# Performance work log

Measured on AMD Instinct MI355X. Metric: run time of the kernel, lower is better.

Reference implementation:

```python
import jax, jax.numpy as jnp
import numpy as np
from jax import lax

KH, KW, K = 3, 3, 9
PAD, BN_EPS = 1, 1e-5


def setup_inputs() -> dict:
    key = jax.random.key(0)
    ks = jax.random.split(key, 10)
    B, CHI, CHO, H, W = 2, 64, 64, 128, 128
    x = jax.random.normal(ks[0], (B, CHI, H, W), dtype=jnp.float32)
    # offset/mask branch conv: 3*K output channels (o1, o2, mask)
    w_off = jax.random.normal(ks[1], (3 * K, CHI, KH, KW), dtype=jnp.float32) * 0.01
    b_off = jax.random.normal(ks[2], (3 * K,), dtype=jnp.float32) * 0.01
    # main deformable conv weight/bias
    fan = CHI * K
    weight = jax.random.normal(ks[3], (CHO, CHI, KH, KW), dtype=jnp.float32) / np.sqrt(fan)
    bias = jax.random.normal(ks[4], (CHO,), dtype=jnp.float32) * 0.01
    # BatchNorm (eval-mode) params
    gamma = jax.random.uniform(ks[5], (CHO,), minval=0.5, maxval=1.5, dtype=jnp.float32)
    beta = jax.random.normal(ks[6], (CHO,), dtype=jnp.float32) * 0.1
    run_mean = jax.random.normal(ks[7], (CHO,), dtype=jnp.float32) * 0.1
    run_var = jax.random.uniform(ks[8], (CHO,), minval=0.5, maxval=1.5, dtype=jnp.float32)
    return {"x": x, "w_off": w_off, "b_off": b_off, "weight": weight,
            "bias": bias, "gamma": gamma, "beta": beta,
            "run_mean": run_mean, "run_var": run_var}


def _dcn_bn_relu(x, w_off, b_off, weight, bias, gamma, beta, run_mean, run_var):
    B, C, H, W = x.shape
    CHO = weight.shape[0]
    # offset/mask branch: regular 3x3 conv, stride 1, pad 1
    om = lax.conv_general_dilated(
        x, w_off, window_strides=(1, 1), padding=[(PAD, PAD), (PAD, PAD)],
        dimension_numbers=("NCHW", "OIHW", "NCHW")) + b_off[None, :, None, None]
    o1, o2, m = jnp.split(om, 3, axis=1)          # each [B, K, H, W]
    offset = jnp.concatenate([o1, o2], axis=1)    # [B, 2K, H, W]
    off_y = offset[:, 0::2]                       # interleaved (y, x) per tap, as in DCNv2 CUDA
    off_x = offset[:, 1::2]
    mask = jax.nn.sigmoid(m)                      # [B, K, H, W] modulation

    # sampling positions: p = p0 + p_k + offset
    ky, kx = jnp.meshgrid(jnp.arange(KH), jnp.arange(KW), indexing="ij")
    ky = ky.reshape(K).astype(x.dtype)
    kx = kx.reshape(K).astype(x.dtype)
    hh = jnp.arange(H, dtype=x.dtype)
    ww = jnp.arange(W, dtype=x.dtype)
    py = hh[None, None, :, None] - PAD + ky[None, :, None, None] + off_y  # [B,K,H,W]
    px = ww[None, None, None, :] - PAD + kx[None, :, None, None] + off_x

    y0f = jnp.floor(py)
    x0f = jnp.floor(px)
    ly = (py - y0f)[..., None]
    lx = (px - x0f)[..., None]
    y0 = y0f.astype(jnp.int32)
    x0 = x0f.astype(jnp.int32)
    bidx = jnp.arange(B)[:, None, None, None]

    def gather(yi, xi):
        valid = ((yi >= 0) & (yi < H) & (xi >= 0) & (xi < W)).astype(x.dtype)
        yc = jnp.clip(yi, 0, H - 1)
        xc = jnp.clip(xi, 0, W - 1)
        g = x[bidx, :, yc, xc]                    # [B, K, H, W, C]
        return g * valid[..., None]

    v00 = gather(y0, x0)
    v01 = gather(y0, x0 + 1)
    v10 = gather(y0 + 1, x0)
    v11 = gather(y0 + 1, x0 + 1)
    sampled = (v00 * (1 - ly) * (1 - lx) + v01 * (1 - ly) * lx
               + v10 * ly * (1 - lx) + v11 * ly * lx)
    sampled = sampled * mask[..., None]           # modulated

    out = jnp.einsum("bkhwc,ock->bohw", sampled,
                     weight.reshape(CHO, C, K)) + bias[None, :, None, None]

    # eval-mode BatchNorm + ReLU
    inv = gamma / jnp.sqrt(run_var + BN_EPS)
    out = (out - run_mean[None, :, None, None]) * inv[None, :, None, None] \
          + beta[None, :, None, None]
    return jax.nn.relu(out)


def reference(x, w_off, b_off, weight, bias, gamma, beta, run_mean, run_var):
    return _dcn_bn_relu(x, w_off, b_off, weight, bias, gamma, beta, run_mean, run_var)
```

## Files before the change

kernel.cpp:

```cpp
#include <hip/hip_runtime.h>
#include <hip/hip_bf16.h>

#define HH 128
#define WW 128
#define CI 64
#define CO 64
#define SLS 584
#define A_HPS 72
#define A_HW 66

typedef __attribute__((ext_vector_type(8))) short short8;
typedef __attribute__((ext_vector_type(4))) float floatx4;

__device__ __forceinline__ unsigned short f2bf(float f) {
  union { float f; unsigned u; } uu; uu.f = f;
  unsigned r = uu.u + 0x7FFFu + ((uu.u >> 16) & 1u);
  return (unsigned short)(r >> 16);
}
__device__ __forceinline__ unsigned pack2bf(float lo, float hi) {
  return (unsigned)f2bf(lo) | ((unsigned)f2bf(hi) << 16);
}

__global__ __launch_bounds__(256) void prep_kernel(
    const float* __restrict__ weight, const float* __restrict__ bias,
    const float* __restrict__ gamma, const float* __restrict__ beta,
    const float* __restrict__ mean, const float* __restrict__ var,
    const float* __restrict__ w_off, const float* __restrict__ b_off,
    unsigned short* __restrict__ Wm, unsigned short* __restrict__ w2,
    float* __restrict__ bias2, float* __restrict__ boff2) {
  int idx = blockIdx.x * 256 + threadIdx.x;
  if (idx < 32) boff2[idx] = (idx < 27) ? b_off[idx] : 0.f;
  if (idx >= CO * 576) return;
  int o = idx / 576, kc = idx - o * 576;
  int k = kc >> 6, c = kc & 63;
  float inv = gamma[o] * rsqrtf(var[o] + 1e-5f);
  Wm[idx] = f2bf(weight[(o * CI + c) * 9 + k] * inv);
  if (kc == 0) bias2[o] = (bias[o] - mean[o]) * inv + beta[o];
  if (o < 27) w2[idx] = f2bf(w_off[o * 576 + c * 9 + k]);
  else if (o < 32) w2[idx] = 0;
}

__global__ __launch_bounds__(256) void offA_kernel(
    const float* __restrict__ x, unsigned* __restrict__ xTb_u,
    const unsigned short* __restrict__ w2, const float* __restrict__ boff2,
    float* __restrict__ om32) {
  __shared__ short halo[3 * A_HW * A_HPS];
  int bid = blockIdx.x;
  int s = bid & 7;
  int n = bid >> 3;
  int b = n >> 5;
  int rest = n & 31;
  int h = s * 16 + (rest & 15);
  int w0 = (rest >> 4) * 64;
  int tid = threadIdx.x;

#pragma unroll
  for (int it = 0; it < 4; it++) {
    int t = it * 256 + tid;
    if (t < 792) {
      int row = t / 264;
      int r2 = t - row * 264;
      int cg4 = r2 / 66;
      int px = r2 - cg4 * 66;
      int y = h - 1 + row;
      int xi = w0 - 1 + px;
      int c0 = cg4 * 16;
      float f[16];
      if (((unsigned)y < (unsigned)HH) && ((unsigned)xi < (unsigned)WW)) {
        const float* xp = x + ((long)(b * CI + c0) * HH + y) * WW + xi;
#pragma unroll
        for (int q = 0; q < 16; q++) f[q] = xp[q * (HH * WW)];
      } else {
#pragma unroll
        for (int q = 0; q < 16; q++) f[q] = 0.f;
      }
      short* hp = &halo[(row * A_HW + px) * A_HPS + c0];
#pragma unroll
      for (int q = 0; q < 4; q++)
        *(uint2*)(hp + q * 4) =
            make_uint2(pack2bf(f[4 * q], f[4 * q + 1]), pack2bf(f[4 * q + 2], f[4 * q + 3]));
    }
  }
  __syncthreads();

  {
    int cp = tid & 31;
    int pw = tid >> 5;
#pragma unroll
    for (int it = 0; it < 8; it++) {
      int px = it * 8 + pw;
      unsigned u = *(const unsigned*)&halo[(A_HW + px + 1) * A_HPS + 2 * cp];
      xTb_u[((b * HH + h) * WW + w0 + px) * 32 + cp] = u;
    }
  }

  int lane = tid & 63, wave = tid >> 6;
  int r16 = lane & 15, quad = lane >> 4;
  int m16 = wave & 1;
  floatx4 binit = *(const floatx4*)(boff2 + m16 * 16 + quad * 4);
  const short* ap = (const short*)(w2 + (m16 * 16 + r16) * 576);
#pragma unroll
  for (int i = 0; i < 2; i++) {
    int nt = (wave >> 1) + 2 * i;
    floatx4 t = binit;
#pragma unroll
    for (int kk = 0; kk < 9; kk++) {
      int dy = kk / 3, dx = kk - 3 * (kk / 3);
      const short* hp = &halo[(dy * A_HW + nt * 16 + r16 + dx) * A_HPS];
      short8 b0 = *(const short8*)(hp + quad * 8);
      short8 b1 = *(const short8*)(hp + 32 + quad * 8);
      short8 a0 = *(const short8*)(ap + kk * 64 + quad * 8);
      short8 a1 = *(const short8*)(ap + kk * 64 + 32 + quad * 8);
      t = __builtin_amdgcn_mfma_f32_16x16x32_bf16(a0, b0, t, 0, 0, 0);
      t = __builtin_amdgcn_mfma_f32_16x16x32_bf16(a1, b1, t, 0, 0, 0);
    }
    float* orow = om32 + (long)((b * HH + h) * WW + w0 + nt * 16 + r16) * 32;
#pragma unroll
    for (int r = 0; r < 4; r++) {
      int oc = m16 * 16 + quad * 4 + r;
      if (oc < 27) orow[oc] = t[r];
    }
  }
}

__global__ __launch_bounds__(256) void dcnB_kernel(
    const unsigned short* __restrict__ xTb, const float* __restrict__ om32,
    const unsigned short* __restrict__ Wm, const float* __restrict__ bias2,
    float* __restrict__ out) {
  __shared__ __hip_bfloat16 SL[16 * SLS];
  __shared__ float4 Pw[144];
  __shared__ int2 Po[144];

  int bid = blockIdx.x;
  int s = bid & 7;
  int n = bid >> 3;
  int b = n >> 7;
  int rem = n & 127;
  int h = s * 16 + (rem >> 3);
  int w0 = (rem & 7) * 16;

  int tid = threadIdx.x, lane = tid & 63, wave = tid >> 6;
  const unsigned short* xb = xTb + b * (HH * WW * CI);
  int rowpix = (b * HH + h) * WW + w0;

  if (lane < 36) {
    int p_loc = (lane * 7282) >> 16;
    int k = lane - p_loc * 9;
    int p = wave * 4 + p_loc;
    const float* ob = om32 + (long)(rowpix + p) * 32;
    float oy = ob[2 * k], ox = ob[2 * k + 1], mm = ob[18 + k];
    float msk = 1.f / (1.f + __expf(-mm));
    int ky = (k * 11) >> 5;
    int kx = k - 3 * ky;
    float py = (float)(h - 1 + ky) + oy;
    float px = (float)(w0 + p - 1 + kx) + ox;
    float y0f = floorf(py), x0f = floorf(px);
    float ly = py - y0f, lx = px - x0f;
    int y0 = (int)y0f, x0 = (int)x0f;
    int y1 = y0 + 1, x1 = x0 + 1;
    float lylx = ly * lx;
    bool y0v = (unsigned)y0 < (unsigned)HH, y1v = (unsigned)y1 < (unsigned)HH;
    bool x0v = (unsigned)x0 < (unsigned)WW, x1v = (unsigned)x1 < (unsigned)WW;
    int yc0 = min(max(y0, 0), HH - 1), yc1 = min(max(y1, 0), HH - 1);
    int xc0 = min(max(x0, 0), WW - 1), xc1 = min(max(x1, 0), WW - 1);
    Pw[p * 9 + k] = make_float4((y0v && x0v) ? (1.f - ly - lx + lylx) * msk : 0.f,
                                (y0v && x1v) ? (lx - lylx) * msk : 0.f,
                                (y1v && x0v) ? (ly - lylx) * msk : 0.f,
                                (y1v && x1v) ? lylx * msk : 0.f);
    int dxs = (xc1 - xc0) * CI;
    int dys = (yc1 - yc0) * WW * CI;
    Po[p * 9 + k] = make_int2((yc0 * WW + xc0) * CI, dxs | (dys << 16));
  }

  int cp = lane & 31, ph = lane >> 5, ch = 2 * cp;
#pragma unroll
  for (int j = 0; j < 2; j++) {
    int p = wave * 4 + j * 2 + ph;
#pragma unroll
    for (int k = 0; k < 9; k++) {
      float4 wv = Pw[p * 9 + k];
      int2 po = Po[p * 9 + k];
      int o00 = po.x + ch;
      int dx = po.y & 0xffff;
      int dyv = po.y >> 16;
      unsigned u00 = *(const unsigned*)(xb + o00);
      unsigned u01 = *(const unsigned*)(xb + o00 + dx);
      unsigned u10 = *(const unsigned*)(xb + o00 + dyv);
      unsigned u11 = *(const unsigned*)(xb + o00 + dyv + dx);
      float lo = __uint_as_float(u00 << 16) * wv.x + __uint_as_float(u01 << 16) * wv.y +
                 __uint_as_float(u10 << 16) * wv.z + __uint_as_float(u11 << 16) * wv.w;
      float hi = __uint_as_float(u00 & 0xffff0000u) * wv.x + __uint_as_float(u01 & 0xffff0000u) * wv.y +
                 __uint_as_float(u10 & 0xffff0000u) * wv.z + __uint_as_float(u11 & 0xffff0000u) * wv.w;
      *(unsigned*)(&SL[p * SLS + k * 64 + ch]) = pack2bf(lo, hi);
    }
  }
  __syncthreads();

  int r16 = lane & 15, quad = lane >> 4;
  floatx4 acc = *(const floatx4*)(bias2 + wave * 16 + quad * 4);
  const unsigned short* Ap = Wm + (wave * 16 + r16) * 576 + quad * 8;
  const __hip_bfloat16* Sp = &SL[r16 * SLS + quad * 8];
#pragma unroll
  for (int kc0 = 0; kc0 < 576; kc0 += 32) {
    short8 av = *(const short8*)(Ap + kc0);
    short8 bv = *(const short8*)(Sp + kc0);
    acc = __builtin_amdgcn_mfma_f32_16x16x32_bf16(av, bv, acc, 0, 0, 0);
  }
#pragma unroll
  for (int r = 0; r < 4; r++) {
    int o = wave * 16 + quad * 4 + r;
    out[((b * CO + o) * HH + h) * WW + w0 + r16] = fmaxf(acc[r], 0.f);
  }
}

extern "C" void kernel_launch(void* const* d_in, const int* in_sizes, int n_in,
                              void* d_out, int out_size, void* d_ws, size_t ws_size,
                              hipStream_t stream) {
  const float* x = (const float*)d_in[0];
  const float* w_off = (const float*)d_in[1];
  const float* b_off = (const float*)d_in[2];
  const float* weight = (const float*)d_in[3];
  const float* bias = (const float*)d_in[4];
  const float* gamma = (const float*)d_in[5];
  const float* beta = (const float*)d_in[6];
  const float* run_mean = (const float*)d_in[7];
  const float* run_var = (const float*)d_in[8];
  float* outp = (float*)d_out;

  char* ws = (char*)d_ws;
  unsigned* xTb = (unsigned*)ws;
  float* om32 = (float*)(ws + 4194304);
  unsigned short* Wm = (unsigned short*)(ws + 8388608);
  unsigned short* w2 = (unsigned short*)(ws + 8462336);
  float* bias2 = (float*)(ws + 8499200);
  float* boff2 = (float*)(ws + 8499456);

  prep_kernel<<<144, 256, 0, stream>>>(weight, bias, gamma, beta, run_mean, run_var,
                                       w_off, b_off, Wm, w2, bias2, boff2);
  offA_kernel<<<512, 256, 0, stream>>>(x, xTb, w2, boff2, om32);
  dcnB_kernel<<<2048, 256, 0, stream>>>((const unsigned short*)xTb, om32, Wm, bias2, outp);
}
```

Measured before the change: 111.9 us.

## Fuse offset conv into DCN kernel and move x transpose into prep kernel

Removes the separate offset-conv kernel and its om32 buffer. The NHWC bf16 transpose of x now runs in extra blocks of the prep kernel through a shared-memory transpose. Each DCN block computes its own 3x3 offset/mask conv on a small 3x18-pixel halo loaded from xTb, splitting K across wave pairs, and keeps the result in shared memory that is aliased with the sampling buffer. This saves a launch and a global round-trip for the offsets, at the cost of recomputing halo loads per 16-pixel tile. The gather is also widened to 4 channels per lane.

After: 117.1 us. 4.6% more time.

```diff
diff --git a/kernel.cpp b/kernel.cpp
--- a/kernel.cpp
+++ b/kernel.cpp
@@ -6,8 +6,8 @@
 #define CI 64
 #define CO 64
 #define SLS 584
-#define A_HPS 72
-#define A_HW 66
+#define HPS 72
+#define HALW 18
 
 typedef __attribute__((ext_vector_type(8))) short short8;
 typedef __attribute__((ext_vector_type(4))) float floatx4;
@@ -20,15 +20,44 @@
 __device__ __forceinline__ unsigned pack2bf(float lo, float hi) {
   return (unsigned)f2bf(lo) | ((unsigned)f2bf(hi) << 16);
 }
+__device__ __forceinline__ float bfl(unsigned u) { return __uint_as_float(u << 16); }
+__device__ __forceinline__ float bfh(unsigned u) { return __uint_as_float(u & 0xffff0000u); }
 
 __global__ __launch_bounds__(256) void prep_kernel(
+    const float* __restrict__ x, unsigned* __restrict__ xTb_u,
     const float* __restrict__ weight, const float* __restrict__ bias,
     const float* __restrict__ gamma, const float* __restrict__ beta,
     const float* __restrict__ mean, const float* __restrict__ var,
     const float* __restrict__ w_off, const float* __restrict__ b_off,
     unsigned short* __restrict__ Wm, unsigned short* __restrict__ w2,
     float* __restrict__ bias2, float* __restrict__ boff2) {
-  int idx = blockIdx.x * 256 + threadIdx.x;
+  __shared__ unsigned T2[128 * 33];
+  int bid = blockIdx.x;
+  int tid = threadIdx.x;
+  if (bid < 256) {
+    int b = bid >> 7, h = bid & 127;
+    int cp = tid >> 3, wc = tid & 7;
+    const float* xp = x + (((long)(b * CI + 2 * cp) * HH + h) * WW + wc * 16);
+#pragma unroll
+    for (int i = 0; i < 4; i++) {
+      float4 a0 = *(const float4*)(xp + i * 4);
+      float4 a1 = *(const float4*)(xp + HH * WW + i * 4);
+      T2[(wc * 16 + i * 4 + 0) * 33 + cp] = pack2bf(a0.x, a1.x);
+      T2[(wc * 16 + i * 4 + 1) * 33 + cp] = pack2bf(a0.y, a1.y);
+      T2[(wc * 16 + i * 4 + 2) * 33 + cp] = pack2bf(a0.z, a1.z);
+      T2[(wc * 16 + i * 4 + 3) * 33 + cp] = pack2bf(a0.w, a1.w);
+    }
+    __syncthreads();
+    int px = tid >> 1, g = tid & 1;
+    const unsigned* src = &T2[px * 33 + g * 16];
+    unsigned* dst = xTb_u + (long)(bid * 128 + px) * 32 + g * 16;
+#pragma unroll
+    for (int q = 0; q < 4; q++)
+      *(uint4*)(dst + 4 * q) =
+          make_uint4(src[4 * q], src[4 * q + 1], src[4 * q + 2], src[4 * q + 3]);
+    return;
+  }
+  int idx = (bid - 256) * 256 + tid;
   if (idx < 32) boff2[idx] = (idx < 27) ? b_off[idx] : 0.f;
   if (idx >= CO * 576) return;
   int o = idx / 576, kc = idx - o * 576;
@@ -40,96 +69,17 @@
   else if (o < 32) w2[idx] = 0;
 }
 
-__global__ __launch_bounds__(256) void offA_kernel(
-    const float* __restrict__ x, unsigned* __restrict__ xTb_u,
+__global__ __launch_bounds__(256) void dcn_kernel(
+    const unsigned short* __restrict__ xTb,
     const unsigned short* __restrict__ w2, const float* __restrict__ boff2,
-    float* __restrict__ om32) {
-  __shared__ short halo[3 * A_HW * A_HPS];
-  int bid = blockIdx.x;
-  int s = bid & 7;
-  int n = bid >> 3;
-  int b = n >> 5;
-  int rest = n & 31;
-  int h = s * 16 + (rest & 15);
-  int w0 = (rest >> 4) * 64;
-  int tid = threadIdx.x;
-
-#pragma unroll
-  for (int it = 0; it < 4; it++) {
-    int t = it * 256 + tid;
-    if (t < 792) {
-      int row = t / 264;
-      int r2 = t - row * 264;
-      int cg4 = r2 / 66;
-      int px = r2 - cg4 * 66;
-      int y = h - 1 + row;
-      int xi = w0 - 1 + px;
-      int c0 = cg4 * 16;
-      float f[16];
-      if (((unsigned)y < (unsigned)HH) && ((unsigned)xi < (unsigned)WW)) {
-        const float* xp = x + ((long)(b * CI + c0) * HH + y) * WW + xi;
-#pragma unroll
-        for (int q = 0; q < 16; q++) f[q] = xp[q * (HH * WW)];
-      } else {
-#pragma unroll
-        for (int q = 0; q < 16; q++) f[q] = 0.f;
-      }
-      short* hp = &halo[(row * A_HW + px) * A_HPS + c0];
-#pragma unroll
-      for (int q = 0; q < 4; q++)
-        *(uint2*)(hp + q * 4) =
-            make_uint2(pack2bf(f[4 * q], f[4 * q + 1]), pack2bf(f[4 * q + 2], f[4 * q + 3]));
-    }
-  }
-  __syncthreads();
-
-  {
-    int cp = tid & 31;
-    int pw = tid >> 5;
-#pragma unroll
-    for (int it = 0; it < 8; it++) {
-      int px = it * 8 + pw;
-      unsigned u = *(const unsigned*)&halo[(A_HW + px + 1) * A_HPS + 2 * cp];
-      xTb_u[((b * HH + h) * WW + w0 + px) * 32 + cp] = u;
-    }
-  }
-
-  int lane = tid & 63, wave = tid >> 6;
-  int r16 = lane & 15, quad = lane >> 4;
-  int m16 = wave & 1;
-  floatx4 binit = *(const floatx4*)(boff2 + m16 * 16 + quad * 4);
-  const short* ap = (const short*)(w2 + (m16 * 16 + r16) * 576);
-#pragma unroll
-  for (int i = 0; i < 2; i++) {
-    int nt = (wave >> 1) + 2 * i;
-    floatx4 t = binit;
-#pragma unroll
-    for (int kk = 0; kk < 9; kk++) {
-      int dy = kk / 3, dx = kk - 3 * (kk / 3);
-      const short* hp = &halo[(dy * A_HW + nt * 16 + r16 + dx) * A_HPS];
-      short8 b0 = *(const short8*)(hp + quad * 8);
-      short8 b1 = *(const short8*)(hp + 32 + quad * 8);
-      short8 a0 = *(const short8*)(ap + kk * 64 + quad * 8);
-      short8 a1 = *(const short8*)(ap + kk * 64 + 32 + quad * 8);
-      t = __builtin_amdgcn_mfma_f32_16x16x32_bf16(a0, b0, t, 0, 0, 0);
-      t = __builtin_amdgcn_mfma_f32_16x16x32_bf16(a1, b1, t, 0, 0, 0);
-    }
-    float* orow = om32 + (long)((b * HH + h) * WW + w0 + nt * 16 + r16) * 32;
-#pragma unroll
-    for (int r = 0; r < 4; r++) {
-      int oc = m16 * 16 + quad * 4 + r;
-      if (oc < 27) orow[oc] = t[r];
-    }
-  }
-}
-
-__global__ __launch_bounds__(256) void dcnB_kernel(
-    const unsigned short* __restrict__ xTb, const float* __restrict__ om32,
     const unsigned short* __restrict__ Wm, const float* __restrict__ bias2,
     float* __restrict__ out) {
-  __shared__ __hip_bfloat16 SL[16 * SLS];
-  __shared__ float4 Pw[144];
-  __shared__ int2 Po[144];
+  __shared__ char smem[26752];
+  short* hal = (short*)smem;
+  __hip_bfloat16* SL = (__hip_bfloat16*)smem;
+  float* omL = (float*)(smem + 18688);
+  float4* Pw = (float4*)(smem + 23296);
+  int2* Po = (int2*)(smem + 25600);
 
   int bid = blockIdx.x;
   int s = bid & 7;
@@ -138,24 +88,57 @@
   int rem = n & 127;
   int h = s * 16 + (rem >> 3);
   int w0 = (rem & 7) * 16;
-
   int tid = threadIdx.x, lane = tid & 63, wave = tid >> 6;
-  const unsigned short* xb = xTb + b * (HH * WW * CI);
-  int rowpix = (b * HH + h) * WW + w0;
+
+#pragma unroll
+  for (int it = 0; it < 2; it++) {
+    int t = it * 256 + tid;
+    if (t < 432) {
+      int row = t / 144;
+      int r2 = t - row * 144;
+      int xi = r2 >> 3, cg = r2 & 7;
+      int y = h - 1 + row, xx = w0 - 1 + xi;
+      uint4 v = make_uint4(0u, 0u, 0u, 0u);
+      if ((unsigned)y < (unsigned)HH && (unsigned)xx < (unsigned)WW)
+        v = *(const uint4*)(xTb + (long)((b * HH + y) * WW + xx) * CI + cg * 8);
+      *(uint4*)(hal + (row * HALW + xi) * HPS + cg * 8) = v;
+    }
+  }
+  __syncthreads();
+
+  {
+    int r16 = lane & 15, quad = lane >> 4;
+    int m16 = wave & 1, kh = wave >> 1;
+    floatx4 t = {0.f, 0.f, 0.f, 0.f};
+    if (kh == 0) t = *(const floatx4*)(boff2 + m16 * 16 + quad * 4);
+    const short* ap = (const short*)(w2 + (m16 * 16 + r16) * 576 + kh * 32 + quad * 8);
+#pragma unroll
+    for (int kk = 0; kk < 9; kk++) {
+      int dy = kk / 3, dxk = kk - 3 * (kk / 3);
+      short8 bfrag = *(const short8*)(hal + (dy * HALW + r16 + dxk) * HPS + kh * 32 + quad * 8);
+      short8 afrag = *(const short8*)(ap + kk * 64);
+      t = __builtin_amdgcn_mfma_f32_16x16x32_bf16(afrag, bfrag, t, 0, 0, 0);
+    }
+    *(floatx4*)(omL + kh * 576 + r16 * 36 + m16 * 16 + quad * 4) = t;
+  }
+  __syncthreads();
 
   if (lane < 36) {
     int p_loc = (lane * 7282) >> 16;
     int k = lane - p_loc * 9;
     int p = wave * 4 + p_loc;
-    const float* ob = om32 + (long)(rowpix + p) * 32;
-    float oy = ob[2 * k], ox = ob[2 * k + 1], mm = ob[18 + k];
+    const float* o0 = omL + p * 36;
+    const float* o1 = omL + 576 + p * 36;
+    float oy = o0[2 * k] + o1[2 * k];
+    float ox = o0[2 * k + 1] + o1[2 * k + 1];
+    float mm = o0[18 + k] + o1[18 + k];
     float msk = 1.f / (1.f + __expf(-mm));
     int ky = (k * 11) >> 5;
     int kx = k - 3 * ky;
     float py = (float)(h - 1 + ky) + oy;
-    float px = (float)(w0 + p - 1 + kx) + ox;
-    float y0f = floorf(py), x0f = floorf(px);
-    float ly = py - y0f, lx = px - x0f;
+    float pxx = (float)(w0 + p - 1 + kx) + ox;
+    float y0f = floorf(py), x0f = floorf(pxx);
+    float ly = py - y0f, lx = pxx - x0f;
     int y0 = (int)y0f, x0 = (int)x0f;
     int y1 = y0 + 1, x1 = x0 + 1;
     float lylx = ly * lx;
@@ -172,44 +155,47 @@
     Po[p * 9 + k] = make_int2((yc0 * WW + xc0) * CI, dxs | (dys << 16));
   }
 
-  int cp = lane & 31, ph = lane >> 5, ch = 2 * cp;
-#pragma unroll
-  for (int j = 0; j < 2; j++) {
-    int p = wave * 4 + j * 2 + ph;
+  {
+    int cq = lane & 15, pl = lane >> 4;
+    int p = wave * 4 + pl;
+    const unsigned short* xb = xTb + (long)b * (HH * WW * CI);
 #pragma unroll
     for (int k = 0; k < 9; k++) {
       float4 wv = Pw[p * 9 + k];
       int2 po = Po[p * 9 + k];
-      int o00 = po.x + ch;
+      int o00 = po.x + cq * 4;
       int dx = po.y & 0xffff;
       int dyv = po.y >> 16;
-      unsigned u00 = *(const unsigned*)(xb + o00);
-      unsigned u01 = *(const unsigned*)(xb + o00 + dx);
-      unsigned u10 = *(const unsigned*)(xb + o00 + dyv);
-      unsigned u11 = *(const unsigned*)(xb + o00 + dyv + dx);
-      float lo = __uint_as_float(u00 << 16) * wv.x + __uint_as_float(u01 << 16) * wv.y +
-                 __uint_as_float(u10 << 16) * wv.z + __uint_as_float(u11 << 16) * wv.w;
-      float hi = __uint_as_float(u00 & 0xffff0000u) * wv.x + __uint_as_float(u01 & 0xffff0000u) * wv.y +
-                 __uint_as_float(u10 & 0xffff0000u) * wv.z + __uint_as_float(u11 & 0xffff0000u) * wv.w;
-      *(unsigned*)(&SL[p * SLS + k * 64 + ch]) = pack2bf(lo, hi);
+      uint2 u00 = *(const uint2*)(xb + o00);
+      uint2 u01 = *(const uint2*)(xb + o00 + dx);
+      uint2 u10 = *(const uint2*)(xb + o00 + dyv);
+      uint2 u11 = *(const uint2*)(xb + o00 + dyv + dx);
+      float lo0 = bfl(u00.x) * wv.x + bfl(u01.x) * wv.y + bfl(u10.x) * wv.z + bfl(u11.x) * wv.w;
+      float hi0 = bfh(u00.x) * wv.x + bfh(u01.x) * wv.y + bfh(u10.x) * wv.z + bfh(u11.x) * wv.w;
+      float lo1 = bfl(u00.y) * wv.x + bfl(u01.y) * wv.y + bfl(u10.y) * wv.z + bfl(u11.y) * wv.w;
+      float hi1 = bfh(u00.y) * wv.x + bfh(u01.y) * wv.y + bfh(u10.y) * wv.z + bfh(u11.y) * wv.w;
+      *(uint2*)(&SL[p * SLS + k * 64 + cq * 4]) =
+          make_uint2(pack2bf(lo0, hi0), pack2bf(lo1, hi1));
     }
   }
   __syncthreads();
 
-  int r16 = lane & 15, quad = lane >> 4;
-  floatx4 acc = *(const floatx4*)(bias2 + wave * 16 + quad * 4);
-  const unsigned short* Ap = Wm + (wave * 16 + r16) * 576 + quad * 8;
-  const __hip_bfloat16* Sp = &SL[r16 * SLS + quad * 8];
-#pragma unroll
-  for (int kc0 = 0; kc0 < 576; kc0 += 32) {
-    short8 av = *(const short8*)(Ap + kc0);
-    short8 bv = *(const short8*)(Sp + kc0);
-    acc = __builtin_amdgcn_mfma_f32_16x16x32_bf16(av, bv, acc, 0, 0, 0);
-  }
-#pragma unroll
-  for (int r = 0; r < 4; r++) {
-    int o = wave * 16 + quad * 4 + r;
-    out[((b * CO + o) * HH + h) * WW + w0 + r16] = fmaxf(acc[r], 0.f);
+  {
+    int r16 = lane & 15, quad = lane >> 4;
+    floatx4 acc = *(const floatx4*)(bias2 + wave * 16 + quad * 4);
+    const unsigned short* Ap = Wm + (wave * 16 + r16) * 576 + quad * 8;
+    const __hip_bfloat16* Sp = &SL[r16 * SLS + quad * 8];
+#pragma unroll
+    for (int kc0 = 0; kc0 < 576; kc0 += 32) {
+      short8 av = *(const short8*)(Ap + kc0);
+      short8 bv = *(const short8*)(Sp + kc0);
+      acc = __builtin_amdgcn_mfma_f32_16x16x32_bf16(av, bv, acc, 0, 0, 0);
+    }
+#pragma unroll
+    for (int r = 0; r < 4; r++) {
+      int o = wave * 16 + quad * 4 + r;
+      out[((b * CO + o) * HH + h) * WW + w0 + r16] = fmaxf(acc[r], 0.f);
+    }
   }
 }
 
@@ -229,14 +215,14 @@
 
   char* ws = (char*)d_ws;
   unsigned* xTb = (unsigned*)ws;
-  float* om32 = (float*)(ws + 4194304);
-  unsigned short* Wm = (unsigned short*)(ws + 8388608);
-  unsigned short* w2 = (unsigned short*)(ws + 8462336);
-  float* bias2 = (float*)(ws + 8499200);
-  float* boff2 = (float*)(ws + 8499456);
-
-  prep_kernel<<<144, 256, 0, stream>>>(weight, bias, gamma, beta, run_mean, run_var,
-                                       w_off, b_off, Wm, w2, bias2, boff2);
-  offA_kernel<<<512, 256, 0, stream>>>(x, xTb, w2, boff2, om32);
-  dcnB_kernel<<<2048, 256, 0, stream>>>((const unsigned short*)xTb, om32, Wm, bias2, outp);
-}
+  unsigned short* Wm = (unsigned short*)(ws + 4194304);
+  unsigned short* w2 = (unsigned short*)(ws + 4268032);
+  float* bias2 = (float*)(ws + 4304896);
+  float* boff2 = (float*)(ws + 4305152);
+
+  prep_kernel<<<400, 256, 0, stream>>>(x, xTb, weight, bias, gamma, beta,
+                                       run_mean, run_var, w_off, b_off,
+                                       Wm, w2, bias2, boff2);
+  dcn_kernel<<<2048, 256, 0, stream>>>((const unsigned short*)xTb, w2, boff2,
+                                       Wm, bias2, outp);
+}
```
